# Kernel optimization log

Measured on AMD Instinct MI355X. Metric: run time of the kernel, lower is better.

Reference implementation:

```python
import jax, jax.numpy as jnp
import numpy as np

N_ITEMS = 1_000_000
T_STEPS = 128
ALPHA = 0.2


def setup_inputs() -> dict:
    key = jax.random.key(0)
    k1, k2 = jax.random.split(key)
    pop_history = jax.random.uniform(k1, (N_ITEMS, T_STEPS), dtype=jnp.float32)
    time = jax.random.randint(k2, (N_ITEMS,), 0, T_STEPS, dtype=jnp.int64 if jax.config.jax_enable_x64 else jnp.int32)
    return {"pop_history": pop_history, "time": time, "item_id": 0}


def _ema(pop_history, alpha):
    # pop_history: [N, T] -> EMA along time axis, ema[:,0] = x[:,0]
    x = pop_history.T  # [T, N]

    def step(carry, xt):
        e = (1.0 - alpha) * carry + alpha * xt
        return e, e

    init = x[0]
    _, rest = jax.lax.scan(step, init, x[1:])  # rest: [T-1, N]
    return jnp.concatenate([init[None, :], rest], axis=0).T  # [N, T]


def reference(pop_history, time, item_id):
    history_ema = _ema(pop_history, ALPHA)                 # [N, T]
    idx = jnp.clip(time - 1, 0)                            # clamp(min=0)
    history_final = jnp.take_along_axis(history_ema, idx[:, None].astype(jnp.int32), axis=1)  # [N, 1]
    return jax.nn.sigmoid(history_final)
```

## Files before the change

kernel.cpp:

```cpp
#include <hip/hip_runtime.h>
#include <hip/hip_bf16.h>


#define T_STEPS 128

__global__ __launch_bounds__(256) void ModulePopHistory_kernel(
    const float* __restrict__ pop,
    const int* __restrict__ timev,
    float* __restrict__ out,
    int n)
{
    int i = blockIdx.x * blockDim.x + threadIdx.x;
    if (i >= n) return;

    int idx = timev[i] - 1;
    if (idx < 0) idx = 0;
    if (idx > T_STEPS - 1) idx = T_STEPS - 1;

    const float4* row = (const float4*)(pop + (size_t)i * T_STEPS);
    int c_last = idx >> 2;
    int rem    = idx & 3;

    float4 w = row[0];
    float ema = w.x;
    if (c_last == 0) {
        if (rem >= 1) ema = fmaf(0.8f, ema, 0.2f * w.y);
        if (rem >= 2) ema = fmaf(0.8f, ema, 0.2f * w.z);
        if (rem >= 3) ema = fmaf(0.8f, ema, 0.2f * w.w);
    } else {
        ema = fmaf(0.8f, ema, 0.2f * w.y);
        ema = fmaf(0.8f, ema, 0.2f * w.z);
        ema = fmaf(0.8f, ema, 0.2f * w.w);

        for (int c = 1; c < c_last; ++c) {
            float4 v = row[c];
            ema = fmaf(0.8f, ema, 0.2f * v.x);
            ema = fmaf(0.8f, ema, 0.2f * v.y);
            ema = fmaf(0.8f, ema, 0.2f * v.z);
            ema = fmaf(0.8f, ema, 0.2f * v.w);
        }

        float4 v = row[c_last];
        ema = fmaf(0.8f, ema, 0.2f * v.x);
        if (rem >= 1) ema = fmaf(0.8f, ema, 0.2f * v.y);
        if (rem >= 2) ema = fmaf(0.8f, ema, 0.2f * v.z);
        if (rem >= 3) ema = fmaf(0.8f, ema, 0.2f * v.w);
    }

    float s = 1.0f / (1.0f + __expf(-ema));
    out[i] = s;
}

extern "C" void kernel_launch(void* const* d_in, const int* in_sizes, int n_in,
                              void* d_out, int out_size, void* d_ws, size_t ws_size,
                              hipStream_t stream) {
    const float* pop = (const float*)d_in[0];
    const int* timev = (const int*)d_in[1];
    float* out = (float*)d_out;

    int n = in_sizes[1];
    const int block = 256;
    int grid = (n + block - 1) / block;
    hipLaunchKernelGGL(ModulePopHistory_kernel, dim3(grid), dim3(block), 0, stream,
                       pop, timev, out, n);
}
```

Measured before the change: 715.1 us.

## Compute EMA as closed-form weighted sum split across 16 lanes per row

Replaces the sequential per-thread EMA recurrence with a closed-form weighted sum. Each of 16 lanes handles 8 timesteps of a row, with weights computed from a power of 0.8 via exp2f, and the partial sums are combined with a shuffle reduction. This removes the long serial FMA chain and makes each wave's row loads contiguous, so coalescing improves and reads past the needed timestep are skipped. The grid becomes a capped grid-stride loop. The power-based weights can differ slightly in floating point from the recurrence.

After: 617.9 us. 13.6% less time.

```diff
diff --git a/kernel.cpp b/kernel.cpp
--- a/kernel.cpp
+++ b/kernel.cpp
@@ -1,5 +1,4 @@
 #include <hip/hip_runtime.h>
-#include <hip/hip_bf16.h>
 
 
 #define T_STEPS 128
@@ -10,45 +9,61 @@
     float* __restrict__ out,
     int n)
 {
-    int i = blockIdx.x * blockDim.x + threadIdx.x;
-    if (i >= n) return;
+    const int lane = threadIdx.x & 63;
+    const int g    = lane >> 4;
+    const int sub  = lane & 15;
+    const int wave = threadIdx.x >> 6;
 
-    int idx = timev[i] - 1;
-    if (idx < 0) idx = 0;
-    if (idx > T_STEPS - 1) idx = T_STEPS - 1;
+    const float L08 = -0.32192809488736234f;
+    const float C1 = 0.25f,        C2 = 0.3125f,       C3 = 0.390625f;
+    const float C4 = 0.48828125f,  C5 = 0.6103515625f, C6 = 0.762939453125f;
+    const float C7 = 0.95367431640625f;
 
-    const float4* row = (const float4*)(pop + (size_t)i * T_STEPS);
-    int c_last = idx >> 2;
-    int rem    = idx & 3;
+    const int t0 = sub * 8;
 
-    float4 w = row[0];
-    float ema = w.x;
-    if (c_last == 0) {
-        if (rem >= 1) ema = fmaf(0.8f, ema, 0.2f * w.y);
-        if (rem >= 2) ema = fmaf(0.8f, ema, 0.2f * w.z);
-        if (rem >= 3) ema = fmaf(0.8f, ema, 0.2f * w.w);
-    } else {
-        ema = fmaf(0.8f, ema, 0.2f * w.y);
-        ema = fmaf(0.8f, ema, 0.2f * w.z);
-        ema = fmaf(0.8f, ema, 0.2f * w.w);
+    for (int base = blockIdx.x * 16; base < n; base += gridDim.x * 16)
+    {
+        const int row   = base + wave * 4 + g;
+        const bool valid = (row < n);
 
-        for (int c = 1; c < c_last; ++c) {
-            float4 v = row[c];
-            ema = fmaf(0.8f, ema, 0.2f * v.x);
-            ema = fmaf(0.8f, ema, 0.2f * v.y);
-            ema = fmaf(0.8f, ema, 0.2f * v.z);
-            ema = fmaf(0.8f, ema, 0.2f * v.w);
+        int idx = 0;
+        if (valid) {
+            idx = timev[row] - 1;
+            if (idx < 0) idx = 0;
         }
 
-        float4 v = row[c_last];
-        ema = fmaf(0.8f, ema, 0.2f * v.x);
-        if (rem >= 1) ema = fmaf(0.8f, ema, 0.2f * v.y);
-        if (rem >= 2) ema = fmaf(0.8f, ema, 0.2f * v.z);
-        if (rem >= 3) ema = fmaf(0.8f, ema, 0.2f * v.w);
+        const int k0 = idx - t0;
+        float acc = 0.0f;
+
+        if (valid && k0 >= 0) {
+            const float4* rp = (const float4*)(pop + (size_t)row * T_STEPS) + sub * 2;
+            const float4 v0 = rp[0];
+            const float p = exp2f((float)k0 * L08);
+
+            const float w0 = (t0 == 0) ? p : 0.2f * p;
+            acc = w0 * v0.x;
+            acc = fmaf((k0 >= 1) ? C1 * p : 0.0f, v0.y, acc);
+            acc = fmaf((k0 >= 2) ? C2 * p : 0.0f, v0.z, acc);
+            acc = fmaf((k0 >= 3) ? C3 * p : 0.0f, v0.w, acc);
+
+            if (k0 >= 4) {
+                const float4 v1 = rp[1];
+                acc = fmaf(C4 * p, v1.x, acc);
+                acc = fmaf((k0 >= 5) ? C5 * p : 0.0f, v1.y, acc);
+                acc = fmaf((k0 >= 6) ? C6 * p : 0.0f, v1.z, acc);
+                acc = fmaf((k0 >= 7) ? C7 * p : 0.0f, v1.w, acc);
+            }
+        }
+
+        acc += __shfl_xor(acc, 1, 64);
+        acc += __shfl_xor(acc, 2, 64);
+        acc += __shfl_xor(acc, 4, 64);
+        acc += __shfl_xor(acc, 8, 64);
+
+        if (valid && sub == 0) {
+            out[row] = 1.0f / (1.0f + __expf(-acc));
+        }
     }
-
-    float s = 1.0f / (1.0f + __expf(-ema));
-    out[i] = s;
 }
 
 extern "C" void kernel_launch(void* const* d_in, const int* in_sizes, int n_in,
@@ -60,7 +75,8 @@
 
     int n = in_sizes[1];
     const int block = 256;
-    int grid = (n + block - 1) / block;
+    int grid = (n + 15) / 16;
+    if (grid > 2048) grid = 2048;
     hipLaunchKernelGGL(ModulePopHistory_kernel, dim3(grid), dim3(block), 0, stream,
                        pop, timev, out, n);
 }
```
